# Optimization experiments

Measured on AMD Instinct MI355X. Metric: run time of the kernel, lower is better.

## Reference

```python
import jax, jax.numpy as jnp
import numpy as np

def setup_inputs() -> dict:
    key = jax.random.key(0)
    k1, k2, k3, k4 = jax.random.split(key, 4)
    B, S, E, H = 4, 4096, 1024, 64
    x = jax.random.normal(k1, (B, S, E), dtype=jnp.float32)
    scale = E ** -0.5  # keep activations well-scaled like trained Linear weights
    Wq = jax.random.normal(k2, (E, H), dtype=jnp.float32) * scale
    Wk = jax.random.normal(k3, (E, H), dtype=jnp.float32) * scale
    Wv = jax.random.normal(k4, (E, H), dtype=jnp.float32) * scale
    return {"x": x, "Wq": Wq, "Wk": Wk, "Wv": Wv}

def reference(x, Wq, Wk, Wv):
    # x: [B, S, E]; W*: [E, H]
    B, S, E = x.shape
    H = Wq.shape[1]
    q = jnp.einsum('bse,eh->bsh', x, Wq)
    k = jnp.einsum('bse,eh->bsh', x, Wk)
    v = jnp.einsum('bse,eh->bsh', x, Wv)
    att = jnp.einsum('bqh,bkh->bqk', q, k) * (H ** -0.5)  # [B, S, S]
    causal = jnp.tril(jnp.ones((S, S), dtype=bool))
    att = jnp.where(causal, att, -jnp.inf)
    att = jax.nn.softmax(att, axis=-1)
    # dropout p=0.0 (eval-mode): identity
    return jnp.einsum('bqk,bkh->bqh', att, v)
```

## Files before the change

### kernel.cpp

```cpp
#include <hip/hip_runtime.h>


using short8 = __attribute__((ext_vector_type(8))) short;
using f32x4  = __attribute__((ext_vector_type(4))) float;

#define MFMA16(A, B, C) __builtin_amdgcn_mfma_f32_16x16x32_bf16((A), (B), (C), 0, 0, 0)

typedef const __attribute__((address_space(1))) void* gas_ptr;
typedef __attribute__((address_space(3))) void*       las_ptr;

__device__ __forceinline__ void gload16(const void* g, void* l) {
    __builtin_amdgcn_global_load_lds((gas_ptr)g, (las_ptr)l, 16, 0, 0);
}

__device__ __forceinline__ unsigned short f2bf(float f) {
    unsigned u = __builtin_bit_cast(unsigned, f);
    u += 0x7fffu + ((u >> 16) & 1u);
    return (unsigned short)(u >> 16);
}
__device__ __forceinline__ float bf2f(unsigned short u) {
    unsigned v = ((unsigned)u) << 16;
    return __builtin_bit_cast(float, v);
}

__device__ __forceinline__ float exp2_fast(float x) {
#if __has_builtin(__builtin_amdgcn_exp2f)
    return __builtin_amdgcn_exp2f(x);
#else
    float r;
    asm("v_exp_f32 %0, %1" : "=v"(r) : "v"(x));
    return r;
#endif
}

__global__ __launch_bounds__(256) void transpose_w(
    const float* __restrict__ Wq,
    const float* __restrict__ Wk,
    const float* __restrict__ Wv,
    unsigned short* __restrict__ Ws)
{
    int o = blockIdx.x * 256 + threadIdx.x;
    if (o < 196608) {
        int j    = o & 7;
        int l    = (o >> 3) & 63;
        int g    = (o >> 9) & 7;
        int rem  = o >> 12;
        int mt   = rem % 3;
        int sk   = rem / 3;
        int c    = g >> 2, nt = g & 3;
        int quad = l >> 4, n  = l & 15;
        int e    = sk * 64 + c * 32 + quad * 8 + j;
        int h    = nt * 16 + n;
        const float* W = (mt == 0) ? Wq : (mt == 1) ? Wk : Wv;
        Ws[o] = f2bf(W[e * 64 + h]);
    }
}

__global__ __launch_bounds__(256, 1) void proj_all(
    const float* __restrict__ x,
    const unsigned short* __restrict__ Ws,
    unsigned short* __restrict__ Qo,
    unsigned short* __restrict__ Ko,
    unsigned short* __restrict__ Vto)
{
    const int m0   = blockIdx.x * 32;
    const int tid  = threadIdx.x;
    const int lane = tid & 63;
    const int wv   = tid >> 6;
    const int rt   = wv & 1;
    const int ch   = wv >> 1;
    const int quad = lane >> 4;
    const int n    = lane & 15;

    __shared__ __align__(16) float xs[3][8][64][4];
    __shared__ __align__(16) short wf[3][24][64][8];

    const f32x4 zero4 = {0.f, 0.f, 0.f, 0.f};
    f32x4 acc[3][2];
    #pragma unroll
    for (int mt = 0; mt < 3; ++mt)
        #pragma unroll
        for (int ntl = 0; ntl < 2; ++ntl) acc[mt][ntl] = zero4;

    auto stage = [&](int t, int qb) {
        int k0 = t * 64;
        #pragma unroll
        for (int it = 0; it < 2; ++it) {
            int i     = wv + 4 * it;
            int chunk = n ^ (quad << 2);
            gload16(x + (size_t)(m0 + 4 * i + quad) * 1024 + k0 + chunk * 4,
                    &xs[qb][i][0][0]);
        }
        #pragma unroll
        for (int it = 0; it < 6; ++it) {
            int f = wv + 4 * it;
            gload16(Ws + (((size_t)t * 24 + f) << 9) + lane * 8, &wf[qb][f][0][0]);
        }
    };

    auto compute = [&](int qb) {
        int sub = n & 3, s = sub << 2;
        const float* xp = &xs[qb][rt * 4 + (n >> 2)][0][0] + sub * 64;
        f32x4 u0 = *(const f32x4*)(xp + (((2 * quad)     ^ s) << 2));
        f32x4 u1 = *(const f32x4*)(xp + (((2 * quad + 1) ^ s) << 2));
        f32x4 u2 = *(const f32x4*)(xp + (((8 + 2 * quad) ^ s) << 2));
        f32x4 u3 = *(const f32x4*)(xp + (((9 + 2 * quad) ^ s) << 2));
        short8 a0, a1;
        #pragma unroll
        for (int j = 0; j < 4; ++j) {
            a0[j]     = (short)f2bf(u0[j]);
            a0[4 + j] = (short)f2bf(u1[j]);
            a1[j]     = (short)f2bf(u2[j]);
            a1[4 + j] = (short)f2bf(u3[j]);
        }
        #pragma unroll
        for (int mt = 0; mt < 3; ++mt)
            #pragma unroll
            for (int ntl = 0; ntl < 2; ++ntl) {
                int nt = 2 * ch + ntl;
                acc[mt][ntl] = MFMA16(a0, *(const short8*)(&wf[qb][mt * 8 + nt][lane][0]),     acc[mt][ntl]);
                acc[mt][ntl] = MFMA16(a1, *(const short8*)(&wf[qb][mt * 8 + 4 + nt][lane][0]), acc[mt][ntl]);
            }
    };

    stage(0, 0);
    stage(1, 1);

    int qb = 0;
    for (int t = 0; t < 15; ++t) {
        asm volatile("s_waitcnt vmcnt(8)" ::: "memory");
        asm volatile("s_waitcnt lgkmcnt(0)" ::: "memory");
        __builtin_amdgcn_s_barrier();
        __builtin_amdgcn_sched_barrier(0);
        if (t < 14) {
            int qn = qb + 2; if (qn >= 3) qn -= 3;
            stage(t + 2, qn);
        }
        compute(qb);
        if (++qb == 3) qb = 0;
    }
    asm volatile("s_waitcnt vmcnt(0)" ::: "memory");
    asm volatile("s_waitcnt lgkmcnt(0)" ::: "memory");
    __builtin_amdgcn_s_barrier();
    __builtin_amdgcn_sched_barrier(0);
    compute(qb);

    #pragma unroll
    for (int ntl = 0; ntl < 2; ++ntl) {
        int h = (2 * ch + ntl) * 16 + n;
        #pragma unroll
        for (int r = 0; r < 4; ++r) {
            int m = m0 + rt * 16 + quad * 4 + r;
            Qo[(size_t)m * 64 + h] = f2bf(acc[0][ntl][r]);
            Ko[(size_t)m * 64 + h] = f2bf(acc[1][ntl][r]);
            int b = m >> 12, s2 = m & 4095;
            Vto[((size_t)(b * 80 + h)) * 4096 + s2] = f2bf(acc[2][ntl][r]);
        }
    }
}

template <int SPLIT>
__device__ __forceinline__ void attn_body(
    const unsigned short* __restrict__ Q,
    const unsigned short* __restrict__ K,
    const unsigned short* __restrict__ Vt,
    float* __restrict__ dst,
    int b, int r0, int kt0, int kt1)
{
    const int tid  = threadIdx.x;
    const int lane = tid & 63;
    const int wv   = tid >> 6;
    const int quad = lane >> 4;
    const int n    = lane & 15;
    const int ktmask = r0 >> 6;

    __shared__ __align__(16) short kf[2][8][64][8];
    __shared__ __align__(16) short vf[2][8][64][8];
    __shared__ __align__(16) unsigned short pbuf[4][32][72];

    short8 qa[2][2];
    #pragma unroll
    for (int rg = 0; rg < 2; ++rg) {
        const unsigned short* qp =
            Q + (size_t)(b * 4096 + r0 + wv * 32 + rg * 16 + n) * 64 + quad * 8;
        #pragma unroll
        for (int j = 0; j < 8; ++j) {
            qa[rg][0][j] = (short)f2bf(bf2f(qp[j])      * 0.18033688f);
            qa[rg][1][j] = (short)f2bf(bf2f(qp[32 + j]) * 0.18033688f);
        }
    }

    const f32x4 zero4 = {0.f, 0.f, 0.f, 0.f};
    f32x4 oacc[2][4];
    float lacc[2][4];
    #pragma unroll
    for (int rg = 0; rg < 2; ++rg)
        #pragma unroll
        for (int nt = 0; nt < 4; ++nt) { oacc[rg][nt] = zero4; lacc[rg][nt] = 0.f; }

    const unsigned short* kbase = K  + ((size_t)b * 4096 + n) * 64 + quad * 8;
    const unsigned short* vbase = Vt + ((size_t)b * 80 + n) * 4096 + quad * 8;

    auto stage = [&](int kt, int p) {
        #pragma unroll
        for (int it = 0; it < 4; ++it) {
            int f = wv + 4 * it;
            if (f < 8) {
                int c = f >> 2, nt = f & 3;
                gload16(kbase + (size_t)(kt * 64 + nt * 16) * 64 + c * 32, &kf[p][f][0][0]);
            } else {
                int pnl = f - 8;
                int nt = pnl >> 1, c = pnl & 1;
                gload16(vbase + (size_t)nt * 16 * 4096 + kt * 64 + c * 32, &vf[p][pnl][0][0]);
            }
        }
    };

    int p = 0;
    stage(kt0, 0);
    __syncthreads();

    for (int kt = kt0; kt <= kt1; ++kt) {
        if (kt < kt1) stage(kt + 1, p ^ 1);

        f32x4 sacc[2][4];
        #pragma unroll
        for (int rg = 0; rg < 2; ++rg)
            #pragma unroll
            for (int nt = 0; nt < 4; ++nt) sacc[rg][nt] = zero4;

        #pragma unroll
        for (int nt = 0; nt < 4; ++nt) {
            short8 ka = *(const short8*)(&kf[p][nt][lane][0]);
            short8 kb = *(const short8*)(&kf[p][4 + nt][lane][0]);
            #pragma unroll
            for (int rg = 0; rg < 2; ++rg) {
                sacc[rg][nt] = MFMA16(qa[rg][0], ka, sacc[rg][nt]);
                sacc[rg][nt] = MFMA16(qa[rg][1], kb, sacc[rg][nt]);
            }
        }

        if (kt >= ktmask) {
            #pragma unroll
            for (int rg = 0; rg < 2; ++rg) {
                int qg = r0 + wv * 32 + rg * 16 + quad * 4;
                #pragma unroll
                for (int nt = 0; nt < 4; ++nt)
                    #pragma unroll
                    for (int r = 0; r < 4; ++r) {
                        int key = kt * 64 + nt * 16 + n;
                        if (key > qg + r) sacc[rg][nt][r] = -1e30f;
                    }
            }
        }

        #pragma unroll
        for (int rg = 0; rg < 2; ++rg)
            #pragma unroll
            for (int r = 0; r < 4; ++r) {
                float rs = 0.f;
                #pragma unroll
                for (int nt = 0; nt < 4; ++nt) {
                    unsigned short pv = f2bf(exp2_fast(sacc[rg][nt][r]));
                    pbuf[wv][rg * 16 + quad * 4 + r][nt * 16 + n] = pv;
                    rs += bf2f(pv);
                }
                lacc[rg][r] += rs;
            }

        short8 pa[2][2];
        #pragma unroll
        for (int rg = 0; rg < 2; ++rg) {
            pa[rg][0] = *(const short8*)(&pbuf[wv][rg * 16 + n][quad * 8]);
            pa[rg][1] = *(const short8*)(&pbuf[wv][rg * 16 + n][32 + quad * 8]);
        }
        #pragma unroll
        for (int nt = 0; nt < 4; ++nt) {
            short8 va = *(const short8*)(&vf[p][2 * nt][lane][0]);
            short8 vb = *(const short8*)(&vf[p][2 * nt + 1][lane][0]);
            #pragma unroll
            for (int rg = 0; rg < 2; ++rg) {
                oacc[rg][nt] = MFMA16(pa[rg][0], va, oacc[rg][nt]);
                oacc[rg][nt] = MFMA16(pa[rg][1], vb, oacc[rg][nt]);
            }
        }

        __syncthreads();
        p ^= 1;
    }

    #pragma unroll
    for (int rg = 0; rg < 2; ++rg)
        #pragma unroll
        for (int r = 0; r < 4; ++r) {
            float v = lacc[rg][r];
            v += __shfl_xor(v, 1);
            v += __shfl_xor(v, 2);
            v += __shfl_xor(v, 4);
            v += __shfl_xor(v, 8);
            lacc[rg][r] = v;
        }

    if (SPLIT) {
        #pragma unroll
        for (int rg = 0; rg < 2; ++rg)
            #pragma unroll
            for (int r = 0; r < 4; ++r) {
                int row = wv * 32 + rg * 16 + quad * 4 + r;
                #pragma unroll
                for (int nt = 0; nt < 4; ++nt)
                    dst[row * 64 + nt * 16 + n] = oacc[rg][nt][r];
                if (n == 0) dst[8192 + row] = lacc[rg][r];
            }
    } else {
        #pragma unroll
        for (int rg = 0; rg < 2; ++rg)
            #pragma unroll
            for (int r = 0; r < 4; ++r) {
                float inv = 1.f / lacc[rg][r];
                int q = r0 + wv * 32 + rg * 16 + quad * 4 + r;
                #pragma unroll
                for (int nt = 0; nt < 4; ++nt)
                    dst[(size_t)(b * 4096 + q) * 64 + nt * 16 + n] = oacc[rg][nt][r] * inv;
            }
    }
}

__global__ __launch_bounds__(256, 3) void attn_part(
    const unsigned short* __restrict__ Q,
    const unsigned short* __restrict__ K,
    const unsigned short* __restrict__ Vt,
    float* __restrict__ Part)
{
    int id = blockIdx.x;
    int b  = id & 3;
    int t  = 143 - (id >> 2);
    int g  = 0;
    while (2 * (g + 1) * (g + 2) <= t) ++g;
    int u  = t - 2 * g * (g + 1);
    int qt = 4 * g + u / (g + 1);
    int c  = u - (u / (g + 1)) * (g + 1);

    int r0  = qt * 128;
    int kt0 = c * 8;
    int kt1 = min(kt0 + 7, 2 * qt + 1);

    float* dst = Part + (size_t)(b * 144 + t) * 8320;
    attn_body<1>(Q, K, Vt, dst, b, r0, kt0, kt1);
}

__global__ __launch_bounds__(256, 3) void attn_mono(
    const unsigned short* __restrict__ Q,
    const unsigned short* __restrict__ K,
    const unsigned short* __restrict__ Vt,
    float* __restrict__ out)
{
    int id = blockIdx.x;
    int qt = 31 - (id >> 2);
    int b  = id & 3;
    attn_body<0>(Q, K, Vt, out, b, qt * 128, 0, 2 * qt + 1);
}

__global__ __launch_bounds__(256) void combine(
    const float* __restrict__ Part, float* __restrict__ out)
{
    int id    = blockIdx.x;
    int slice = id & 7;
    int bq    = id >> 3;
    int b     = bq & 3;
    int qt    = bq >> 2;
    int g     = qt >> 2;
    int nc    = g + 1;
    int t0    = 2 * g * (g + 1) + (qt & 3) * (g + 1);
    const float* P0 = Part + (size_t)(b * 144 + t0) * 8320;

    int tid = threadIdx.x;

    __shared__ float invden[16];
    if (tid < 16) {
        float d[8] = {0, 0, 0, 0, 0, 0, 0, 0};
        #pragma unroll 8
        for (int c = 0; c < 8; ++c)
            if (c < nc) d[c] = P0[c * 8320 + 8192 + slice * 16 + tid];
        invden[tid] = 1.f / (((d[0] + d[1]) + (d[2] + d[3])) +
                             ((d[4] + d[5]) + (d[6] + d[7])));
    }

    float acc[4] = {0, 0, 0, 0};
    const float* Pe = P0 + slice * 1024 + tid;
    for (int c = 0; c < nc; ++c) {
        const float* Pc = Pe + (size_t)c * 8320;
        #pragma unroll
        for (int j = 0; j < 4; ++j)
            acc[j] += Pc[j * 256];
    }

    __syncthreads();
    #pragma unroll
    for (int j = 0; j < 4; ++j) {
        int e   = j * 256 + tid;
        int row = e >> 6;
        out[((size_t)b * 4096 + qt * 128 + slice * 16) * 64 + (size_t)e]
            = acc[j] * invden[row];
    }
}

extern "C" void kernel_launch(void* const* d_in, const int* in_sizes, int n_in,
                              void* d_out, int out_size, void* d_ws, size_t ws_size,
                              hipStream_t stream) {
    const float* x  = (const float*)d_in[0];
    const float* Wq = (const float*)d_in[1];
    const float* Wk = (const float*)d_in[2];
    const float* Wv = (const float*)d_in[3];
    float* outp = (float*)d_out;
    unsigned short* ws = (unsigned short*)d_ws;

    unsigned short* Qw  = ws;
    unsigned short* Kw  = ws + 1048576;
    unsigned short* Vtw = ws + 2097152;
    unsigned short* Wsp = ws + 3407872;

    size_t part_off = ((size_t)3604480 * 2 + 255) & ~(size_t)255;
    size_t need     = part_off + (size_t)4 * 144 * 8320 * 4;
    float* Part = (float*)((char*)d_ws + part_off);

    transpose_w<<<dim3(768), dim3(256), 0, stream>>>(Wq, Wk, Wv, Wsp);
    proj_all<<<dim3(512), dim3(256), 0, stream>>>(x, Wsp, Qw, Kw, Vtw);

    if (ws_size >= need) {
        attn_part<<<dim3(576), dim3(256), 0, stream>>>(Qw, Kw, Vtw, Part);
        combine<<<dim3(1024), dim3(256), 0, stream>>>(Part, outp);
    } else {
        attn_mono<<<dim3(128), dim3(256), 0, stream>>>(Qw, Kw, Vtw, outp);
    }
}
```

Baseline: 156.1 us.

## Load projection weight fragments directly from global and cut LDS for occupancy

The QKV projection kernel no longer stages the pre-swizzled bf16 weight fragments through LDS. Each wave loads its weight fragments directly from global memory (served by cache) and now owns one 16-column tile across both row groups. The x tile staging drops from triple to double buffering with plain __syncthreads, and the launch bounds allow three blocks per CU. The goal is to cut LDS footprint and synchronisation cost so more blocks fit per CU. The trade-off is more global/L2 weight traffic per block and a shallower pipeline with less latency hiding.

```diff
diff --git a/kernel.cpp b/kernel.cpp
--- a/kernel.cpp
+++ b/kernel.cpp
@@ -56,7 +56,7 @@
     }
 }
 
-__global__ __launch_bounds__(256, 1) void proj_all(
+__global__ __launch_bounds__(256, 3) void proj_all(
     const float* __restrict__ x,
     const unsigned short* __restrict__ Ws,
     unsigned short* __restrict__ Qo,
@@ -66,95 +66,82 @@
     const int m0   = blockIdx.x * 32;
     const int tid  = threadIdx.x;
     const int lane = tid & 63;
-    const int wv   = tid >> 6;
-    const int rt   = wv & 1;
-    const int ch   = wv >> 1;
+    const int ch   = tid >> 6;
     const int quad = lane >> 4;
     const int n    = lane & 15;
 
-    __shared__ __align__(16) float xs[3][8][64][4];
-    __shared__ __align__(16) short wf[3][24][64][8];
+    __shared__ __align__(16) float xs[2][8][64][4];
 
     const f32x4 zero4 = {0.f, 0.f, 0.f, 0.f};
     f32x4 acc[3][2];
     #pragma unroll
     for (int mt = 0; mt < 3; ++mt)
         #pragma unroll
-        for (int ntl = 0; ntl < 2; ++ntl) acc[mt][ntl] = zero4;
-
-    auto stage = [&](int t, int qb) {
+        for (int rg = 0; rg < 2; ++rg) acc[mt][rg] = zero4;
+
+    auto stage = [&](int t, int p) {
         int k0 = t * 64;
         #pragma unroll
         for (int it = 0; it < 2; ++it) {
-            int i     = wv + 4 * it;
+            int i     = ch + 4 * it;
             int chunk = n ^ (quad << 2);
             gload16(x + (size_t)(m0 + 4 * i + quad) * 1024 + k0 + chunk * 4,
-                    &xs[qb][i][0][0]);
-        }
-        #pragma unroll
-        for (int it = 0; it < 6; ++it) {
-            int f = wv + 4 * it;
-            gload16(Ws + (((size_t)t * 24 + f) << 9) + lane * 8, &wf[qb][f][0][0]);
+                    &xs[p][i][0][0]);
         }
     };
 
-    auto compute = [&](int qb) {
-        int sub = n & 3, s = sub << 2;
-        const float* xp = &xs[qb][rt * 4 + (n >> 2)][0][0] + sub * 64;
-        f32x4 u0 = *(const f32x4*)(xp + (((2 * quad)     ^ s) << 2));
-        f32x4 u1 = *(const f32x4*)(xp + (((2 * quad + 1) ^ s) << 2));
-        f32x4 u2 = *(const f32x4*)(xp + (((8 + 2 * quad) ^ s) << 2));
-        f32x4 u3 = *(const f32x4*)(xp + (((9 + 2 * quad) ^ s) << 2));
-        short8 a0, a1;
-        #pragma unroll
-        for (int j = 0; j < 4; ++j) {
-            a0[j]     = (short)f2bf(u0[j]);
-            a0[4 + j] = (short)f2bf(u1[j]);
-            a1[j]     = (short)f2bf(u2[j]);
-            a1[4 + j] = (short)f2bf(u3[j]);
-        }
-        #pragma unroll
-        for (int mt = 0; mt < 3; ++mt)
-            #pragma unroll
-            for (int ntl = 0; ntl < 2; ++ntl) {
-                int nt = 2 * ch + ntl;
-                acc[mt][ntl] = MFMA16(a0, *(const short8*)(&wf[qb][mt * 8 + nt][lane][0]),     acc[mt][ntl]);
-                acc[mt][ntl] = MFMA16(a1, *(const short8*)(&wf[qb][mt * 8 + 4 + nt][lane][0]), acc[mt][ntl]);
-            }
-    };
-
     stage(0, 0);
-    stage(1, 1);
-
-    int qb = 0;
-    for (int t = 0; t < 15; ++t) {
-        asm volatile("s_waitcnt vmcnt(8)" ::: "memory");
-        asm volatile("s_waitcnt lgkmcnt(0)" ::: "memory");
-        __builtin_amdgcn_s_barrier();
-        __builtin_amdgcn_sched_barrier(0);
-        if (t < 14) {
-            int qn = qb + 2; if (qn >= 3) qn -= 3;
-            stage(t + 2, qn);
-        }
-        compute(qb);
-        if (++qb == 3) qb = 0;
-    }
-    asm volatile("s_waitcnt vmcnt(0)" ::: "memory");
-    asm volatile("s_waitcnt lgkmcnt(0)" ::: "memory");
-    __builtin_amdgcn_s_barrier();
-    __builtin_amdgcn_sched_barrier(0);
-    compute(qb);
-
-    #pragma unroll
-    for (int ntl = 0; ntl < 2; ++ntl) {
-        int h = (2 * ch + ntl) * 16 + n;
+    __syncthreads();
+
+    int p = 0;
+    for (int t = 0; t < 16; ++t) {
+        if (t < 15) stage(t + 1, p ^ 1);
+
+        const unsigned short* wp = Ws + (((size_t)t * 24) << 9) + (size_t)lane * 8;
+        short8 w0[3], w1[3];
+        #pragma unroll
+        for (int mt = 0; mt < 3; ++mt) {
+            w0[mt] = *(const short8*)(wp + ((size_t)(mt * 8 + ch)     << 9));
+            w1[mt] = *(const short8*)(wp + ((size_t)(mt * 8 + 4 + ch) << 9));
+        }
+
+        #pragma unroll
+        for (int rg = 0; rg < 2; ++rg) {
+            int sub = n & 3, s = sub << 2;
+            const float* xp = &xs[p][rg * 4 + (n >> 2)][0][0] + sub * 64;
+            f32x4 u0 = *(const f32x4*)(xp + (((2 * quad)     ^ s) << 2));
+            f32x4 u1 = *(const f32x4*)(xp + (((2 * quad + 1) ^ s) << 2));
+            f32x4 u2 = *(const f32x4*)(xp + (((8 + 2 * quad) ^ s) << 2));
+            f32x4 u3 = *(const f32x4*)(xp + (((9 + 2 * quad) ^ s) << 2));
+            short8 a0, a1;
+            #pragma unroll
+            for (int j = 0; j < 4; ++j) {
+                a0[j]     = (short)f2bf(u0[j]);
+                a0[4 + j] = (short)f2bf(u1[j]);
+                a1[j]     = (short)f2bf(u2[j]);
+                a1[4 + j] = (short)f2bf(u3[j]);
+            }
+            #pragma unroll
+            for (int mt = 0; mt < 3; ++mt) {
+                acc[mt][rg] = MFMA16(a0, w0[mt], acc[mt][rg]);
+                acc[mt][rg] = MFMA16(a1, w1[mt], acc[mt][rg]);
+            }
+        }
+
+        __syncthreads();
+        p ^= 1;
+    }
+
+    const int h = ch * 16 + n;
+    #pragma unroll
+    for (int rg = 0; rg < 2; ++rg) {
         #pragma unroll
         for (int r = 0; r < 4; ++r) {
-            int m = m0 + rt * 16 + quad * 4 + r;
-            Qo[(size_t)m * 64 + h] = f2bf(acc[0][ntl][r]);
-            Ko[(size_t)m * 64 + h] = f2bf(acc[1][ntl][r]);
+            int m = m0 + rg * 16 + quad * 4 + r;
+            Qo[(size_t)m * 64 + h] = f2bf(acc[0][rg][r]);
+            Ko[(size_t)m * 64 + h] = f2bf(acc[1][rg][r]);
             int b = m >> 12, s2 = m & 4095;
-            Vto[((size_t)(b * 80 + h)) * 4096 + s2] = f2bf(acc[2][ntl][r]);
+            Vto[((size_t)(b * 80 + h)) * 4096 + s2] = f2bf(acc[2][rg][r]);
         }
     }
 }
```

New measurement: 141.8 us. 9.2% less time.
